# Optimization experiments

Hardware: AMD Instinct MI355X
Metric: run time of the kernel (lower is better)

The kernel has to match this reference:

```python
import jax, jax.numpy as jnp
import numpy as np

B, D_IN, H, N_LAYERS, D_OUT = 262144, 8, 128, 3, 1


def setup_inputs() -> dict:
    key = jax.random.key(0)
    ks = jax.random.split(key, 18)
    rn = lambda k, shape, fan: (jax.random.normal(k, shape, jnp.float32) / np.sqrt(fan))
    return {
        "x": jax.random.normal(ks[0], (B, D_IN), jnp.float32),
        "Sw_w": rn(ks[1], (D_IN, H), D_IN),
        "Sw_b": rn(ks[2], (H,), D_IN),
        "Uz": rn(ks[3], (N_LAYERS, D_IN, H), D_IN),
        "Wsz_w": rn(ks[4], (N_LAYERS, H, H), H),
        "Wsz_b": rn(ks[5], (N_LAYERS, H), H),
        "Ug": rn(ks[6], (N_LAYERS, D_IN, H), D_IN),
        "Wsg_w": rn(ks[7], (N_LAYERS, H, H), H),
        "Wsg_b": rn(ks[8], (N_LAYERS, H), H),
        "Ur": rn(ks[9], (N_LAYERS, D_IN, H), D_IN),
        "Wsr_w": rn(ks[10], (N_LAYERS, H, H), H),
        "Wsr_b": rn(ks[11], (N_LAYERS, H), H),
        "Uh": rn(ks[12], (N_LAYERS, D_IN, H), D_IN),
        "Wsh_w": rn(ks[13], (N_LAYERS, H, H), H),
        "Wsh_b": rn(ks[14], (N_LAYERS, H), H),
        "Wf_w": rn(ks[15], (H, D_OUT), H),
        "Wf_b": rn(ks[16], (D_OUT,), H),
    }


def reference(x, Sw_w, Sw_b, Uz, Wsz_w, Wsz_b, Ug, Wsg_w, Wsg_b,
              Ur, Wsr_w, Wsr_b, Uh, Wsh_w, Wsh_b, Wf_w, Wf_b):
    # x: [B, D_in]; S: [B, H]
    S = x @ Sw_w + Sw_b
    n = Uz.shape[0]
    for i in range(n):  # small fixed layer count
        S = jax.nn.sigmoid(S)
        Z = jax.nn.sigmoid(x @ Uz[i] + S @ Wsz_w[i] + Wsz_b[i])
        G = jax.nn.sigmoid(x @ Ug[i] + S @ Wsg_w[i] + Wsg_b[i])
        R = jax.nn.sigmoid(x @ Ur[i] + S @ Wsr_w[i] + Wsr_b[i])
        H_ = jnp.tanh(x @ Uh[i] + (S * R) @ Wsh_w[i] + Wsh_b[i])
        S = (1.0 - G) * H_ + Z * S
    return S @ Wf_w + Wf_b  # [B, D_out]
```

## Files before the change

kernel.cpp:

```cpp
#include <hip/hip_runtime.h>

typedef __bf16 bf16_t;
typedef __bf16 bf16x2 __attribute__((ext_vector_type(2)));
typedef __bf16 bf16x8 __attribute__((ext_vector_type(8)));
typedef float f32x4 __attribute__((ext_vector_type(4)));

#define NL 3
#define HD 128
#define ROWS 64
#define STR 136
#define THREADS 512
#define BATCH 262144
#define NBLK (BATCH / ROWS)

#define SW_OFF 0
#define U_OFF  4096
#define W_OFF  53248
#define WS_ELEMS 249856

#define MFMA(a, b, c) __builtin_amdgcn_mfma_f32_16x16x32_bf16((a), (b), (c), 0, 0, 0)

#define LOG2E 1.4426950408889634f
__device__ __forceinline__ float sigm(float v) {
    return __builtin_amdgcn_rcpf(1.f + __builtin_amdgcn_exp2f(-LOG2E * v));
}
__device__ __forceinline__ float sigmn(float v) {
    return __builtin_amdgcn_rcpf(1.f + __builtin_amdgcn_exp2f(LOG2E * v));
}
__device__ __forceinline__ float tanh_f(float v) {
    return 1.f - 2.f * __builtin_amdgcn_rcpf(__builtin_amdgcn_exp2f((2.f * LOG2E) * v) + 1.f);
}

__global__ void dgm_prep(const float* __restrict__ SwW,
                         const float* __restrict__ Uz, const float* __restrict__ Wz,
                         const float* __restrict__ Ug, const float* __restrict__ Wg,
                         const float* __restrict__ Ur, const float* __restrict__ Wr,
                         const float* __restrict__ Uh, const float* __restrict__ Wh,
                         bf16_t* __restrict__ ws) {
    int idx = blockIdx.x * 256 + threadIdx.x;
    if (idx >= WS_ELEMS) return;
    const float* Us[4] = {Uz, Ug, Ur, Uh};
    const float* Wm[4] = {Wz, Wg, Wr, Wh};
    if (idx < U_OFF) {
        int ct = idx >> 9, rem = idx & 511, lane = rem >> 3, j = rem & 7;
        int q = lane >> 4, mm = lane & 15;
        int k = q * 8 + j, n = ct * 16 + mm;
        ws[idx] = (k < 8) ? (bf16_t)SwW[k * HD + n] : (bf16_t)0.f;
    } else if (idx < W_OFF) {
        int t = idx - U_OFF;
        int lg = t >> 12, r2 = t & 4095;
        int l = lg >> 2, g = lg & 3;
        int ct = r2 >> 9, rem = r2 & 511, lane = rem >> 3, j = rem & 7;
        int q = lane >> 4, mm = lane & 15;
        int k = q * 8 + j, n = ct * 16 + mm;
        ws[idx] = (k < 8) ? (bf16_t)Us[g][(l * 8 + k) * HD + n] : (bf16_t)0.f;
    } else {
        int t = idx - W_OFF;
        int lg = t >> 14, r2 = t & 16383;
        int l = lg >> 2, g = lg & 3;
        int ct = r2 >> 11, kc = (r2 >> 9) & 3, rem = r2 & 511, lane = rem >> 3, j = rem & 7;
        int q = lane >> 4, mm = lane & 15;
        int k = kc * 32 + q * 8 + j, n = ct * 16 + mm;
        ws[idx] = (bf16_t)Wm[g][(l * HD + k) * HD + n];
    }
}

__device__ __forceinline__ f32x4 gate_mm(const bf16_t* abase, const bf16x8* fW, bf16x8 fU) {
    f32x4 acc = {0.f, 0.f, 0.f, 0.f};
#pragma unroll
    for (int kc = 0; kc < 4; kc++) {
        bf16x8 a = *(const bf16x8*)(abase + kc * 32);
        acc = MFMA(a, fW[kc], acc);
    }
    bf16x8 ax = *(const bf16x8*)(abase - ((reinterpret_cast<uintptr_t>(abase) / 2) % STR) + 0);
    return acc;
}

__global__ __launch_bounds__(THREADS, 4) void dgm_main(
    const float* __restrict__ x,
    const float* __restrict__ Swb,
    const float* __restrict__ Bz, const float* __restrict__ Bg,
    const float* __restrict__ Br, const float* __restrict__ Bh,
    const float* __restrict__ WfW, const float* __restrict__ WfB,
    const bf16_t* __restrict__ ws,
    float* __restrict__ out) {
    __shared__ __align__(16) bf16_t s_sig[2][ROWS * STR];
    __shared__ __align__(16) bf16_t s_r[ROWS * STR];
    __shared__ float red[ROWS];

    const int tid = threadIdx.x;
    const int lane = tid & 63;
    const int ct = tid >> 6;
    const int m = lane & 15, q = lane >> 4;
    const int rb = blockIdx.x * ROWS;
    const int c = ct * 16 + m;
    const int fragoff = (ct * 64 + lane) * 8;

    if (tid < ROWS) red[tid] = 0.f;

    {
        int r = tid >> 3, j = tid & 7;
        bf16_t xv = (bf16_t)x[(size_t)(rb + r) * 8 + j];
        s_sig[0][r * STR + 128 + j] = xv;
        s_sig[1][r * STR + 128 + j] = xv;
        s_r[r * STR + 128 + j] = xv;
    }
    __syncthreads();

    {
        const float swb = Swb[c];
        bf16x8 fSw = *(const bf16x8*)(ws + SW_OFF + fragoff);
#pragma unroll
        for (int rt = 0; rt < 4; rt++) {
            bf16x8 a = *(const bf16x8*)(&s_sig[0][(rt * 16 + m) * STR + 128]);
            f32x4 acc = {0.f, 0.f, 0.f, 0.f};
            acc = MFMA(a, fSw, acc);
#pragma unroll
            for (int i = 0; i < 4; i++)
                s_sig[0][(rt * 16 + q * 4 + i) * STR + c] = (bf16_t)sigm(acc[i] + swb);
        }
    }
    __syncthreads();

#pragma unroll 1
    for (int l = 0; l < NL; l++) {
        const int cur = l & 1, nxt = cur ^ 1;
        const bf16_t* wb = ws + W_OFF + (size_t)l * 4 * 16384;
        const bf16_t* ub = ws + U_OFF + (size_t)l * 4 * 4096;

        {
            bf16x8 fU = *(const bf16x8*)(ub + 2 * 4096 + fragoff);
            bf16x8 fW[4];
#pragma unroll
            for (int kc = 0; kc < 4; kc++)
                fW[kc] = *(const bf16x8*)(wb + 2 * 16384 + (ct * 4 + kc) * 512 + lane * 8);
            const float br = Br[l * HD + c];
#pragma unroll
            for (int rt = 0; rt < 4; rt++) {
                const bf16_t* abase = &s_sig[cur][(rt * 16 + m) * STR];
                f32x4 aR = {0.f, 0.f, 0.f, 0.f};
#pragma unroll
                for (int kc = 0; kc < 4; kc++) {
                    bf16x8 a = *(const bf16x8*)(abase + kc * 32 + q * 8);
                    aR = MFMA(a, fW[kc], aR);
                }
                {
                    bf16x8 a = *(const bf16x8*)(abase + 128);
                    aR = MFMA(a, fU, aR);
                }
#pragma unroll
                for (int i = 0; i < 4; i++) {
                    int r = rt * 16 + q * 4 + i;
                    float sb = (float)s_sig[cur][r * STR + c];
                    s_r[r * STR + c] = (bf16_t)(sigm(aR[i] + br) * sb);
                }
            }
        }
        __syncthreads();

        bf16x2 t1p[4][2];
        bf16x2 ogp[4][2];

        {
            bf16x8 fU = *(const bf16x8*)(ub + 0 * 4096 + fragoff);
            bf16x8 fW[4];
#pragma unroll
            for (int kc = 0; kc < 4; kc++)
                fW[kc] = *(const bf16x8*)(wb + 0 * 16384 + (ct * 4 + kc) * 512 + lane * 8);
            const float bz = Bz[l * HD + c];
#pragma unroll
            for (int rt = 0; rt < 4; rt++) {
                const bf16_t* abase = &s_sig[cur][(rt * 16 + m) * STR];
                f32x4 aZ = {0.f, 0.f, 0.f, 0.f};
#pragma unroll
                for (int kc = 0; kc < 4; kc++) {
                    bf16x8 a = *(const bf16x8*)(abase + kc * 32 + q * 8);
                    aZ = MFMA(a, fW[kc], aZ);
                }
                {
                    bf16x8 a = *(const bf16x8*)(abase + 128);
                    aZ = MFMA(a, fU, aZ);
                }
#pragma unroll
                for (int i = 0; i < 4; i++) {
                    int r = rt * 16 + q * 4 + i;
                    float sb = (float)s_sig[cur][r * STR + c];
                    t1p[rt][i >> 1][i & 1] = (bf16_t)(sigm(aZ[i] + bz) * sb);
                }
            }
        }

        {
            bf16x8 fU = *(const bf16x8*)(ub + 1 * 4096 + fragoff);
            bf16x8 fW[4];
#pragma unroll
            for (int kc = 0; kc < 4; kc++)
                fW[kc] = *(const bf16x8*)(wb + 1 * 16384 + (ct * 4 + kc) * 512 + lane * 8);
            const float bg = Bg[l * HD + c];
#pragma unroll
            for (int rt = 0; rt < 4; rt++) {
                const bf16_t* abase = &s_sig[cur][(rt * 16 + m) * STR];
                f32x4 aG = {0.f, 0.f, 0.f, 0.f};
#pragma unroll
                for (int kc = 0; kc < 4; kc++) {
                    bf16x8 a = *(const bf16x8*)(abase + kc * 32 + q * 8);
                    aG = MFMA(a, fW[kc], aG);
                }
                {
                    bf16x8 a = *(const bf16x8*)(abase + 128);
                    aG = MFMA(a, fU, aG);
                }
#pragma unroll
                for (int i = 0; i < 4; i++)
                    ogp[rt][i >> 1][i & 1] = (bf16_t)sigmn(aG[i] + bg);
            }
        }

        {
            bf16x8 fU = *(const bf16x8*)(ub + 3 * 4096 + fragoff);
            bf16x8 fW[4];
#pragma unroll
            for (int kc = 0; kc < 4; kc++)
                fW[kc] = *(const bf16x8*)(wb + 3 * 16384 + (ct * 4 + kc) * 512 + lane * 8);
            const float bh = Bh[l * HD + c];
            const bool last = (l == NL - 1);
            const float wfc = WfW[c];
#pragma unroll
            for (int rt = 0; rt < 4; rt++) {
                const bf16_t* abase = &s_r[(rt * 16 + m) * STR];
                f32x4 aH = {0.f, 0.f, 0.f, 0.f};
#pragma unroll
                for (int kc = 0; kc < 4; kc++) {
                    bf16x8 a = *(const bf16x8*)(abase + kc * 32 + q * 8);
                    aH = MFMA(a, fW[kc], aH);
                }
                {
                    bf16x8 a = *(const bf16x8*)(abase + 128);
                    aH = MFMA(a, fU, aH);
                }
#pragma unroll
                for (int i = 0; i < 4; i++) {
                    int r = rt * 16 + q * 4 + i;
                    float hh = tanh_f(aH[i] + bh);
                    float sn = (float)ogp[rt][i >> 1][i & 1] * hh + (float)t1p[rt][i >> 1][i & 1];
                    if (last) {
                        float p = sn * wfc;
                        p += __shfl_xor(p, 1);
                        p += __shfl_xor(p, 2);
                        p += __shfl_xor(p, 4);
                        p += __shfl_xor(p, 8);
                        if (m == 0) atomicAdd(&red[r], p);
                    } else {
                        s_sig[nxt][r * STR + c] = (bf16_t)sigm(sn);
                    }
                }
            }
        }
        __syncthreads();
    }

    if (tid < ROWS) out[rb + tid] = red[tid] + WfB[0];
}

extern "C" void kernel_launch(void* const* d_in, const int* in_sizes, int n_in,
                              void* d_out, int out_size, void* d_ws, size_t ws_size,
                              hipStream_t stream) {
    const float* x   = (const float*)d_in[0];
    const float* SwW = (const float*)d_in[1];
    const float* Swb = (const float*)d_in[2];
    const float* Uz  = (const float*)d_in[3];
    const float* Wz  = (const float*)d_in[4];
    const float* Bz  = (const float*)d_in[5];
    const float* Ug  = (const float*)d_in[6];
    const float* Wg  = (const float*)d_in[7];
    const float* Bg  = (const float*)d_in[8];
    const float* Ur  = (const float*)d_in[9];
    const float* Wr  = (const float*)d_in[10];
    const float* Br  = (const float*)d_in[11];
    const float* Uh  = (const float*)d_in[12];
    const float* Wh  = (const float*)d_in[13];
    const float* Bh  = (const float*)d_in[14];
    const float* WfW = (const float*)d_in[15];
    const float* WfB = (const float*)d_in[16];
    bf16_t* ws = (bf16_t*)d_ws;
    float* out = (float*)d_out;

    if (ws_size < (size_t)WS_ELEMS * sizeof(bf16_t)) return;

    dgm_prep<<<(WS_ELEMS + 255) / 256, 256, 0, stream>>>(SwW, Uz, Wz, Ug, Wg, Ur, Wr, Uh, Wh, ws);
    dgm_main<<<NBLK, THREADS, 0, stream>>>(x, Swb, Bz, Bg, Br, Bh, WfW, WfB, ws, out);
}
```

Measured before the change: 311.8 us.

## Shrink block to 32 rows with each wave computing two column tiles

The block shrinks from 64 rows and 512 threads to 32 rows and 256 threads. Each wave now computes two 16-column tiles, so every A fragment read from LDS feeds two MFMAs. The sigmoid state is also kept in registers (svp) instead of being re-read from shared memory for the S*R and Z*S products, and the unused gate_mm helper is removed. In exchange, each wave loads twice as many weight fragments from global memory and uses more registers, which may lower occupancy. Weight traffic per row also rises because each block now serves half as many rows.

Result: slower. 547.4 us (+75.5%).

```diff
diff --git a/kernel.cpp b/kernel.cpp
--- a/kernel.cpp
+++ b/kernel.cpp
@@ -7,9 +7,9 @@
 
 #define NL 3
 #define HD 128
-#define ROWS 64
+#define ROWS 32
 #define STR 136
-#define THREADS 512
+#define THREADS 256
 #define BATCH 262144
 #define NBLK (BATCH / ROWS)
 
@@ -65,17 +65,6 @@
     }
 }
 
-__device__ __forceinline__ f32x4 gate_mm(const bf16_t* abase, const bf16x8* fW, bf16x8 fU) {
-    f32x4 acc = {0.f, 0.f, 0.f, 0.f};
-#pragma unroll
-    for (int kc = 0; kc < 4; kc++) {
-        bf16x8 a = *(const bf16x8*)(abase + kc * 32);
-        acc = MFMA(a, fW[kc], acc);
-    }
-    bf16x8 ax = *(const bf16x8*)(abase - ((reinterpret_cast<uintptr_t>(abase) / 2) % STR) + 0);
-    return acc;
-}
-
 __global__ __launch_bounds__(THREADS, 4) void dgm_main(
     const float* __restrict__ x,
     const float* __restrict__ Swb,
@@ -90,11 +79,12 @@
 
     const int tid = threadIdx.x;
     const int lane = tid & 63;
-    const int ct = tid >> 6;
+    const int wv = tid >> 6;
+    const int ct0 = wv, ct1 = wv + 4;
     const int m = lane & 15, q = lane >> 4;
     const int rb = blockIdx.x * ROWS;
-    const int c = ct * 16 + m;
-    const int fragoff = (ct * 64 + lane) * 8;
+    const int c0 = ct0 * 16 + m, c1 = ct1 * 16 + m;
+    const int fo0 = (ct0 * 64 + lane) * 8, fo1 = (ct1 * 64 + lane) * 8;
 
     if (tid < ROWS) red[tid] = 0.f;
 
@@ -107,17 +97,28 @@
     }
     __syncthreads();
 
+    bf16x2 svp[2][2][2];
+
     {
-        const float swb = Swb[c];
-        bf16x8 fSw = *(const bf16x8*)(ws + SW_OFF + fragoff);
-#pragma unroll
-        for (int rt = 0; rt < 4; rt++) {
+        const float swb0 = Swb[c0], swb1 = Swb[c1];
+        bf16x8 fS0 = *(const bf16x8*)(ws + SW_OFF + fo0);
+        bf16x8 fS1 = *(const bf16x8*)(ws + SW_OFF + fo1);
+#pragma unroll
+        for (int rt = 0; rt < 2; rt++) {
             bf16x8 a = *(const bf16x8*)(&s_sig[0][(rt * 16 + m) * STR + 128]);
-            f32x4 acc = {0.f, 0.f, 0.f, 0.f};
-            acc = MFMA(a, fSw, acc);
-#pragma unroll
-            for (int i = 0; i < 4; i++)
-                s_sig[0][(rt * 16 + q * 4 + i) * STR + c] = (bf16_t)sigm(acc[i] + swb);
+            f32x4 a0 = {0.f, 0.f, 0.f, 0.f}, a1 = {0.f, 0.f, 0.f, 0.f};
+            a0 = MFMA(a, fS0, a0);
+            a1 = MFMA(a, fS1, a1);
+#pragma unroll
+            for (int i = 0; i < 4; i++) {
+                int r = rt * 16 + q * 4 + i;
+                bf16_t s0 = (bf16_t)sigm(a0[i] + swb0);
+                bf16_t s1 = (bf16_t)sigm(a1[i] + swb1);
+                svp[rt][0][i >> 1][i & 1] = s0;
+                svp[rt][1][i >> 1][i & 1] = s1;
+                s_sig[0][r * STR + c0] = s0;
+                s_sig[0][r * STR + c1] = s1;
+            }
         }
     }
     __syncthreads();
@@ -129,129 +130,157 @@
         const bf16_t* ub = ws + U_OFF + (size_t)l * 4 * 4096;
 
         {
-            bf16x8 fU = *(const bf16x8*)(ub + 2 * 4096 + fragoff);
-            bf16x8 fW[4];
-#pragma unroll
-            for (int kc = 0; kc < 4; kc++)
-                fW[kc] = *(const bf16x8*)(wb + 2 * 16384 + (ct * 4 + kc) * 512 + lane * 8);
-            const float br = Br[l * HD + c];
-#pragma unroll
-            for (int rt = 0; rt < 4; rt++) {
+            bf16x8 fU0 = *(const bf16x8*)(ub + 2 * 4096 + fo0);
+            bf16x8 fU1 = *(const bf16x8*)(ub + 2 * 4096 + fo1);
+            bf16x8 fW0[4], fW1[4];
+#pragma unroll
+            for (int kc = 0; kc < 4; kc++) {
+                fW0[kc] = *(const bf16x8*)(wb + 2 * 16384 + (ct0 * 4 + kc) * 512 + lane * 8);
+                fW1[kc] = *(const bf16x8*)(wb + 2 * 16384 + (ct1 * 4 + kc) * 512 + lane * 8);
+            }
+            const float br0 = Br[l * HD + c0], br1 = Br[l * HD + c1];
+#pragma unroll
+            for (int rt = 0; rt < 2; rt++) {
                 const bf16_t* abase = &s_sig[cur][(rt * 16 + m) * STR];
-                f32x4 aR = {0.f, 0.f, 0.f, 0.f};
+                f32x4 a0 = {0.f, 0.f, 0.f, 0.f}, a1 = {0.f, 0.f, 0.f, 0.f};
 #pragma unroll
                 for (int kc = 0; kc < 4; kc++) {
                     bf16x8 a = *(const bf16x8*)(abase + kc * 32 + q * 8);
-                    aR = MFMA(a, fW[kc], aR);
+                    a0 = MFMA(a, fW0[kc], a0);
+                    a1 = MFMA(a, fW1[kc], a1);
                 }
                 {
                     bf16x8 a = *(const bf16x8*)(abase + 128);
-                    aR = MFMA(a, fU, aR);
+                    a0 = MFMA(a, fU0, a0);
+                    a1 = MFMA(a, fU1, a1);
                 }
 #pragma unroll
                 for (int i = 0; i < 4; i++) {
                     int r = rt * 16 + q * 4 + i;
-                    float sb = (float)s_sig[cur][r * STR + c];
-                    s_r[r * STR + c] = (bf16_t)(sigm(aR[i] + br) * sb);
+                    s_r[r * STR + c0] = (bf16_t)(sigm(a0[i] + br0) * (float)svp[rt][0][i >> 1][i & 1]);
+                    s_r[r * STR + c1] = (bf16_t)(sigm(a1[i] + br1) * (float)svp[rt][1][i >> 1][i & 1]);
                 }
             }
         }
         __syncthreads();
 
-        bf16x2 t1p[4][2];
-        bf16x2 ogp[4][2];
+        bf16x2 t1p[2][2][2];
+        bf16x2 ogp[2][2][2];
 
         {
-            bf16x8 fU = *(const bf16x8*)(ub + 0 * 4096 + fragoff);
-            bf16x8 fW[4];
-#pragma unroll
-            for (int kc = 0; kc < 4; kc++)
-                fW[kc] = *(const bf16x8*)(wb + 0 * 16384 + (ct * 4 + kc) * 512 + lane * 8);
-            const float bz = Bz[l * HD + c];
-#pragma unroll
-            for (int rt = 0; rt < 4; rt++) {
+            bf16x8 fU0 = *(const bf16x8*)(ub + 0 * 4096 + fo0);
+            bf16x8 fU1 = *(const bf16x8*)(ub + 0 * 4096 + fo1);
+            bf16x8 fW0[4], fW1[4];
+#pragma unroll
+            for (int kc = 0; kc < 4; kc++) {
+                fW0[kc] = *(const bf16x8*)(wb + 0 * 16384 + (ct0 * 4 + kc) * 512 + lane * 8);
+                fW1[kc] = *(const bf16x8*)(wb + 0 * 16384 + (ct1 * 4 + kc) * 512 + lane * 8);
+            }
+            const float bz0 = Bz[l * HD + c0], bz1 = Bz[l * HD + c1];
+#pragma unroll
+            for (int rt = 0; rt < 2; rt++) {
                 const bf16_t* abase = &s_sig[cur][(rt * 16 + m) * STR];
-                f32x4 aZ = {0.f, 0.f, 0.f, 0.f};
+                f32x4 a0 = {0.f, 0.f, 0.f, 0.f}, a1 = {0.f, 0.f, 0.f, 0.f};
 #pragma unroll
                 for (int kc = 0; kc < 4; kc++) {
                     bf16x8 a = *(const bf16x8*)(abase + kc * 32 + q * 8);
-                    aZ = MFMA(a, fW[kc], aZ);
+                    a0 = MFMA(a, fW0[kc], a0);
+                    a1 = MFMA(a, fW1[kc], a1);
                 }
                 {
                     bf16x8 a = *(const bf16x8*)(abase + 128);
-                    aZ = MFMA(a, fU, aZ);
+                    a0 = MFMA(a, fU0, a0);
+                    a1 = MFMA(a, fU1, a1);
+                }
+#pragma unroll
+                for (int i = 0; i < 4; i++) {
+                    t1p[rt][0][i >> 1][i & 1] = (bf16_t)(sigm(a0[i] + bz0) * (float)svp[rt][0][i >> 1][i & 1]);
+                    t1p[rt][1][i >> 1][i & 1] = (bf16_t)(sigm(a1[i] + bz1) * (float)svp[rt][1][i >> 1][i & 1]);
+                }
+            }
+        }
+
+        {
+            bf16x8 fU0 = *(const bf16x8*)(ub + 1 * 4096 + fo0);
+            bf16x8 fU1 = *(const bf16x8*)(ub + 1 * 4096 + fo1);
+            bf16x8 fW0[4], fW1[4];
+#pragma unroll
+            for (int kc = 0; kc < 4; kc++) {
+                fW0[kc] = *(const bf16x8*)(wb + 1 * 16384 + (ct0 * 4 + kc) * 512 + lane * 8);
+                fW1[kc] = *(const bf16x8*)(wb + 1 * 16384 + (ct1 * 4 + kc) * 512 + lane * 8);
+            }
+            const float bg0 = Bg[l * HD + c0], bg1 = Bg[l * HD + c1];
+#pragma unroll
+            for (int rt = 0; rt < 2; rt++) {
+                const bf16_t* abase = &s_sig[cur][(rt * 16 + m) * STR];
+                f32x4 a0 = {0.f, 0.f, 0.f, 0.f}, a1 = {0.f, 0.f, 0.f, 0.f};
+#pragma unroll
+                for (int kc = 0; kc < 4; kc++) {
+                    bf16x8 a = *(const bf16x8*)(abase + kc * 32 + q * 8);
+                    a0 = MFMA(a, fW0[kc], a0);
+                    a1 = MFMA(a, fW1[kc], a1);
+                }
+                {
+                    bf16x8 a = *(const bf16x8*)(abase + 128);
+                    a0 = MFMA(a, fU0, a0);
+                    a1 = MFMA(a, fU1, a1);
+                }
+#pragma unroll
+                for (int i = 0; i < 4; i++) {
+                    ogp[rt][0][i >> 1][i & 1] = (bf16_t)sigmn(a0[i] + bg0);
+                    ogp[rt][1][i >> 1][i & 1] = (bf16_t)sigmn(a1[i] + bg1);
+                }
+            }
+        }
+
+        {
+            bf16x8 fU0 = *(const bf16x8*)(ub + 3 * 4096 + fo0);
+            bf16x8 fU1 = *(const bf16x8*)(ub + 3 * 4096 + fo1);
+            bf16x8 fW0[4], fW1[4];
+#pragma unroll
+            for (int kc = 0; kc < 4; kc++) {
+                fW0[kc] = *(const bf16x8*)(wb + 3 * 16384 + (ct0 * 4 + kc) * 512 + lane * 8);
+                fW1[kc] = *(const bf16x8*)(wb + 3 * 16384 + (ct1 * 4 + kc) * 512 + lane * 8);
+            }
+            const float bh0 = Bh[l * HD + c0], bh1 = Bh[l * HD + c1];
+            const bool last = (l == NL - 1);
+            const float wf0 = WfW[c0], wf1 = WfW[c1];
+#pragma unroll
+            for (int rt = 0; rt < 2; rt++) {
+                const bf16_t* abase = &s_r[(rt * 16 + m) * STR];
+                f32x4 a0 = {0.f, 0.f, 0.f, 0.f}, a1 = {0.f, 0.f, 0.f, 0.f};
+#pragma unroll
+                for (int kc = 0; kc < 4; kc++) {
+                    bf16x8 a = *(const bf16x8*)(abase + kc * 32 + q * 8);
+                    a0 = MFMA(a, fW0[kc], a0);
+                    a1 = MFMA(a, fW1[kc], a1);
+                }
+                {
+                    bf16x8 a = *(const bf16x8*)(abase + 128);
+                    a0 = MFMA(a, fU0, a0);
+                    a1 = MFMA(a, fU1, a1);
                 }
 #pragma unroll
                 for (int i = 0; i < 4; i++) {
                     int r = rt * 16 + q * 4 + i;
-                    float sb = (float)s_sig[cur][r * STR + c];
-                    t1p[rt][i >> 1][i & 1] = (bf16_t)(sigm(aZ[i] + bz) * sb);
-                }
-            }
-        }
-
-        {
-            bf16x8 fU = *(const bf16x8*)(ub + 1 * 4096 + fragoff);
-            bf16x8 fW[4];
-#pragma unroll
-            for (int kc = 0; kc < 4; kc++)
-                fW[kc] = *(const bf16x8*)(wb + 1 * 16384 + (ct * 4 + kc) * 512 + lane * 8);
-            const float bg = Bg[l * HD + c];
-#pragma unroll
-            for (int rt = 0; rt < 4; rt++) {
-                const bf16_t* abase = &s_sig[cur][(rt * 16 + m) * STR];
-                f32x4 aG = {0.f, 0.f, 0.f, 0.f};
-#pragma unroll
-                for (int kc = 0; kc < 4; kc++) {
-                    bf16x8 a = *(const bf16x8*)(abase + kc * 32 + q * 8);
-                    aG = MFMA(a, fW[kc], aG);
-                }
-                {
-                    bf16x8 a = *(const bf16x8*)(abase + 128);
-                    aG = MFMA(a, fU, aG);
-                }
-#pragma unroll
-                for (int i = 0; i < 4; i++)
-                    ogp[rt][i >> 1][i & 1] = (bf16_t)sigmn(aG[i] + bg);
-            }
-        }
-
-        {
-            bf16x8 fU = *(const bf16x8*)(ub + 3 * 4096 + fragoff);
-            bf16x8 fW[4];
-#pragma unroll
-            for (int kc = 0; kc < 4; kc++)
-                fW[kc] = *(const bf16x8*)(wb + 3 * 16384 + (ct * 4 + kc) * 512 + lane * 8);
-            const float bh = Bh[l * HD + c];
-            const bool last = (l == NL - 1);
-            const float wfc = WfW[c];
-#pragma unroll
-            for (int rt = 0; rt < 4; rt++) {
-                const bf16_t* abase = &s_r[(rt * 16 + m) * STR];
-                f32x4 aH = {0.f, 0.f, 0.f, 0.f};
-#pragma unroll
-                for (int kc = 0; kc < 4; kc++) {
-                    bf16x8 a = *(const bf16x8*)(abase + kc * 32 + q * 8);
-                    aH = MFMA(a, fW[kc], aH);
-                }
-                {
-                    bf16x8 a = *(const bf16x8*)(abase + 128);
-                    aH = MFMA(a, fU, aH);
-                }
-#pragma unroll
-                for (int i = 0; i < 4; i++) {
-                    int r = rt * 16 + q * 4 + i;
-                    float hh = tanh_f(aH[i] + bh);
-                    float sn = (float)ogp[rt][i >> 1][i & 1] * hh + (float)t1p[rt][i >> 1][i & 1];
+                    float h0 = tanh_f(a0[i] + bh0);
+                    float h1 = tanh_f(a1[i] + bh1);
+                    float sn0 = (float)ogp[rt][0][i >> 1][i & 1] * h0 + (float)t1p[rt][0][i >> 1][i & 1];
+                    float sn1 = (float)ogp[rt][1][i >> 1][i & 1] * h1 + (float)t1p[rt][1][i >> 1][i & 1];
                     if (last) {
-                        float p = sn * wfc;
-                        p += __shfl_xor(p, 1);
-                        p += __shfl_xor(p, 2);
-                        p += __shfl_xor(p, 4);
-                        p += __shfl_xor(p, 8);
-                        if (m == 0) atomicAdd(&red[r], p);
+                        float p0 = sn0 * wf0, p1 = sn1 * wf1;
+                        p0 += __shfl_xor(p0, 1);  p1 += __shfl_xor(p1, 1);
+                        p0 += __shfl_xor(p0, 2);  p1 += __shfl_xor(p1, 2);
+                        p0 += __shfl_xor(p0, 4);  p1 += __shfl_xor(p1, 4);
+                        p0 += __shfl_xor(p0, 8);  p1 += __shfl_xor(p1, 8);
+                        if (m == 0) atomicAdd(&red[r], p0 + p1);
                     } else {
-                        s_sig[nxt][r * STR + c] = (bf16_t)sigm(sn);
+                        bf16_t s20 = (bf16_t)sigm(sn0);
+                        bf16_t s21 = (bf16_t)sigm(sn1);
+                        svp[rt][0][i >> 1][i & 1] = s20;
+                        svp[rt][1][i >> 1][i & 1] = s21;
+                        s_sig[nxt][r * STR + c0] = s20;
+                        s_sig[nxt][r * STR + c1] = s21;
                     }
                 }
             }
```
